# Kernel optimization log

Hardware: AMD Instinct MI355X
Metric: run time of the kernel (lower is better)

## Reference

```python
import math
import jax, jax.numpy as jnp
import numpy as np

D_MODEL = 896
N_HEADS = 14
D_HEAD = D_MODEL // N_HEADS  # 64
ROPE_BASE = 10000.0
LN_EPS = 1e-5
B, N = 8, 1024


def setup_inputs() -> dict:
    key = jax.random.key(0)
    ks = jax.random.split(key, 12)
    s = 1.0 / math.sqrt(D_MODEL)
    return {
        "node_features": jax.random.normal(ks[0], (B, N, D_MODEL), jnp.float32),
        "adj": jax.random.uniform(ks[1], (N, N), jnp.float32),
        "wind_dirs": jax.random.uniform(ks[2], (B, N), jnp.float32),
        "bearings": jax.random.uniform(ks[3], (N, N), jnp.float32),
        "Wq": jax.random.normal(ks[4], (D_MODEL, D_MODEL), jnp.float32) * s,
        "Wk": jax.random.normal(ks[5], (D_MODEL, D_MODEL), jnp.float32) * s,
        "Wv": jax.random.normal(ks[6], (D_MODEL, D_MODEL), jnp.float32) * s,
        "Wo": jax.random.normal(ks[7], (D_MODEL, D_MODEL), jnp.float32) * s,
        "ln_g": jnp.ones((D_MODEL,), jnp.float32),
        "ln_b": jnp.zeros((D_MODEL,), jnp.float32),
        "wind_w": jax.random.normal(ks[8], (2, N_HEADS), jnp.float32) * (1.0 / math.sqrt(2.0)),
        "wind_b": jnp.zeros((N_HEADS,), jnp.float32),
    }


def _layernorm(x, g, b):
    mu = jnp.mean(x, axis=-1, keepdims=True)
    var = jnp.var(x, axis=-1, keepdims=True)
    return (x - mu) * jax.lax.rsqrt(var + LN_EPS) * g + b


def _apply_rotary(x, cos_h, sin_h):
    # x: (B,H,N,d_head); cos_h/sin_h: (N, d_head//2)
    d_half = x.shape[-1] // 2
    x1, x2 = x[..., :d_half], x[..., d_half:]
    return jnp.concatenate([x1 * cos_h - x2 * sin_h, x2 * cos_h + x1 * sin_h], axis=-1)


def reference(node_features, adj, wind_dirs, bearings, Wq, Wk, Wv, Wo, ln_g, ln_b, wind_w, wind_b):
    Bb, Nn, D = node_features.shape
    residual = node_features
    x = _layernorm(node_features, ln_g, ln_b)

    def proj(W):
        return (x @ W).reshape(Bb, Nn, N_HEADS, D_HEAD).transpose(0, 2, 1, 3)  # (B,H,N,dh)

    Q, K, V = proj(Wq), proj(Wk), proj(Wv)

    # RoPE: cos/sin halves (first d_half entries of the duplicated freq table)
    inv_freq = 1.0 / (ROPE_BASE ** (jnp.arange(0, D_HEAD, 2, dtype=jnp.float32) / D_HEAD))
    freqs = jnp.arange(Nn, dtype=jnp.float32)[:, None] * inv_freq[None, :]  # (N, dh/2)
    cos_h, sin_h = jnp.cos(freqs), jnp.sin(freqs)
    Q = _apply_rotary(Q, cos_h, sin_h)
    K = _apply_rotary(K, cos_h, sin_h)

    attn = jnp.einsum("bhqd,bhkd->bhqk", Q, K) / math.sqrt(D_HEAD)
    adj_mask = (adj > 0)[None, None, :, :]
    attn = jnp.where(adj_mask, attn, -1e30)

    # wind-direction dynamic edge bias
    reverse_bearings = (bearings.T + 180.0) % 360.0  # (N,N)
    alignment = jnp.cos(jnp.deg2rad(wind_dirs[:, :, None] - reverse_bearings[None]))  # (B,N,N)
    dist_feat = jnp.broadcast_to(adj[None], (Bb, Nn, Nn))
    edge_features = jnp.stack([alignment, dist_feat], axis=-1)  # (B,N,N,2)
    wind_bias = jnp.tanh(edge_features @ wind_w + wind_b)  # (B,N,N,H)
    attn = attn + wind_bias.transpose(0, 3, 1, 2)  # (B,H,N,N)

    attn = jax.nn.softmax(attn, axis=-1)  # dropout is identity in eval
    out = jnp.einsum("bhqk,bhkd->bhqd", attn, V)
    out = out.transpose(0, 2, 1, 3).reshape(Bb, Nn, D) @ Wo
    return residual + out
```

## Files before the change

### kernel.cpp

```cpp
#include <hip/hip_runtime.h>
#include <hip/hip_bf16.h>
#include <math.h>

#define B_ 8
#define N_ 1024
#define H_ 14
#define DH_ 64
#define D_ 896
#define M_ (B_*N_)
#define DQKV_ 2688

#define TWO_LOG2E_ 2.8853900817779268f
#define BIAS_C_   (-15.869645449778597f)
#define QSCALE_     0.18033688011112043f
#define RAD_        0.017453292519943295f

typedef __attribute__((ext_vector_type(8))) short bf16x8;
typedef __attribute__((ext_vector_type(4))) short bf16x4;
typedef __attribute__((ext_vector_type(4))) float f32x4;

__device__ __forceinline__ float bf2f(short s){
  unsigned u = ((unsigned)(unsigned short)s) << 16;
  union { unsigned u; float f; } c; c.u = u; return c.f;
}
__device__ __forceinline__ short f2bf(float f){
  union { float f; unsigned u; } c; c.f = f;
  unsigned u = c.u;
  unsigned r = (u + 0x7FFFu + ((u >> 16) & 1u)) >> 16;
  return (short)(unsigned short)r;
}
__device__ __forceinline__ float asf(unsigned u){
  union { unsigned u; float f; } c; c.u = u; return c.f;
}
__device__ __forceinline__ unsigned cvt_pk_bf16(float lo, float hi){
  unsigned r;
  asm("v_cvt_pk_bf16_f32 %0, %1, %2" : "=v"(r) : "v"(lo), "v"(hi));
  return r;
}

#if __has_builtin(__builtin_amdgcn_mfma_f32_16x16x16bf16_1k)
#define MFMA16(D, A, B) (D) = __builtin_amdgcn_mfma_f32_16x16x16bf16_1k((A), (B), (D), 0, 0, 0)
#else
#define MFMA16(D, A, B) asm("v_mfma_f32_16x16x16_bf16 %0, %1, %2, %0" : "+v"(D) : "v"(A), "v"(B))
#endif

#define BAR_LDS() do { asm volatile("s_waitcnt lgkmcnt(0)" ::: "memory"); \
                       __builtin_amdgcn_s_barrier(); } while (0)

__global__ __launch_bounds__(256) void ln_kernel(const float* __restrict__ x,
                                                 const float* __restrict__ g,
                                                 const float* __restrict__ bb,
                                                 short* __restrict__ y)
{
  int row = blockIdx.x;
  const float* xr = x + (size_t)row * D_;
  float s = 0.f, s2 = 0.f;
  for (int i = threadIdx.x; i < D_; i += 256){
    float v = xr[i]; s += v; s2 = fmaf(v, v, s2);
  }
  #pragma unroll
  for (int off = 32; off > 0; off >>= 1){
    s  += __shfl_down(s,  off, 64);
    s2 += __shfl_down(s2, off, 64);
  }
  __shared__ float rs_[4], rs2_[4];
  int wv = threadIdx.x >> 6;
  if ((threadIdx.x & 63) == 0){ rs_[wv] = s; rs2_[wv] = s2; }
  __syncthreads();
  float ts  = rs_[0] + rs_[1] + rs_[2] + rs_[3];
  float ts2 = rs2_[0] + rs2_[1] + rs2_[2] + rs2_[3];
  float mu  = ts * (1.f / D_);
  float var = ts2 * (1.f / D_) - mu * mu;
  float rstd = rsqrtf(var + 1e-5f);
  short* yr = y + (size_t)row * D_;
  for (int i = threadIdx.x; i < D_; i += 256){
    yr[i] = f2bf((xr[i] - mu) * rstd * g[i] + bb[i]);
  }
}

__global__ __launch_bounds__(256) void transpose_kernel(
    const float* __restrict__ Wq, const float* __restrict__ Wk,
    const float* __restrict__ Wv, const float* __restrict__ Wo,
    short* __restrict__ WqkvT, short* __restrict__ WoT)
{
  __shared__ short t[64][72];
  int z = blockIdx.z;
  const float* W = (z == 0) ? Wq : (z == 1) ? Wk : (z == 2) ? Wv : Wo;
  int kb = blockIdx.x * 64, nb = blockIdx.y * 64;
  int c0 = (threadIdx.x & 7) * 8;
  int r0 = threadIdx.x >> 3;
  #pragma unroll
  for (int rr = 0; rr < 64; rr += 32){
    const float* src = &W[(size_t)(kb + r0 + rr) * D_ + nb + c0];
    float4 a = *(const float4*)src;
    float4 b = *(const float4*)(src + 4);
    short* dstl = &t[r0 + rr][c0];
    dstl[0] = f2bf(a.x); dstl[1] = f2bf(a.y); dstl[2] = f2bf(a.z); dstl[3] = f2bf(a.w);
    dstl[4] = f2bf(b.x); dstl[5] = f2bf(b.y); dstl[6] = f2bf(b.z); dstl[7] = f2bf(b.w);
  }
  __syncthreads();
  short* dst = (z < 3) ? (WqkvT + (size_t)(z * D_) * D_) : WoT;
  #pragma unroll
  for (int rr = 0; rr < 64; rr += 32){
    int n = nb + r0 + rr;
    bf16x8 v;
    #pragma unroll
    for (int j = 0; j < 8; j++) v[j] = t[c0 + j][r0 + rr];
    *(bf16x8*)&dst[(size_t)n * D_ + kb + c0] = v;
  }
}

__global__ __launch_bounds__(256) void prep_kernel(
    const float* __restrict__ brg, const float* __restrict__ wdir,
    unsigned* __restrict__ csb, short* __restrict__ alignQ, int do_align)
{
  int kt = blockIdx.x, qt = blockIdx.y;
  __shared__ float brgS[64][65];
  __shared__ float cA_[8][64], sA_[8][64];
  int r  = threadIdx.x >> 2;
  int c0 = (threadIdx.x & 3) * 16;

  float bb[16];
  {
    const float* bp = brg + (size_t)(kt * 64 + r) * N_ + qt * 64 + c0;
    #pragma unroll
    for (int i = 0; i < 16; i += 4){
      float4 bv = *(const float4*)(bp + i);
      bb[i] = bv.x; bb[i+1] = bv.y; bb[i+2] = bv.z; bb[i+3] = bv.w;
    }
  }

  if (do_align){
    #pragma unroll
    for (int i = 0; i < 16; i++) brgS[r][c0 + i] = bb[i];
    for (int idx = threadIdx.x; idx < 512; idx += 256){
      int b = idx >> 6, qq = idx & 63;
      float A = wdir[(size_t)b * N_ + qt * 64 + qq] * RAD_;
      float s, c; __sincosf(A, &s, &c);
      sA_[b][qq] = s; cA_[b][qq] = c;
    }
    __syncthreads();
    float cB[16], sB[16];
    #pragma unroll
    for (int i = 0; i < 16; i++){
      float Br = (brgS[c0 + i][r] + 180.f) * RAD_;
      __sincosf(Br, &sB[i], &cB[i]);
    }
    #pragma unroll
    for (int b = 0; b < 8; b++){
      float ca = cA_[b][r], sa = sA_[b][r];
      unsigned w8[8];
      #pragma unroll
      for (int p = 0; p < 8; p++){
        float a0 = fmaf(ca, cB[2*p],     sa * sB[2*p]);
        float a1 = fmaf(ca, cB[2*p + 1], sa * sB[2*p + 1]);
        w8[p] = cvt_pk_bf16(a0, a1);
      }
      short* dst = alignQ + ((size_t)b * N_ + qt * 64 + r) * N_ + kt * 64 + c0;
      *(uint4*)dst       = make_uint4(w8[0], w8[1], w8[2], w8[3]);
      *(uint4*)(dst + 8) = make_uint4(w8[4], w8[5], w8[6], w8[7]);
    }
  } else {
    unsigned* cp = csb + (size_t)(kt * 64 + r) * N_ + qt * 64 + c0;
    #pragma unroll
    for (int i = 0; i < 16; i += 4){
      unsigned o[4];
      #pragma unroll
      for (int j = 0; j < 4; j++){
        float Br = (bb[i + j] + 180.f) * RAD_;
        float sBv, cBv; __sincosf(Br, &sBv, &cBv);
        o[j] = ((unsigned)(unsigned short)f2bf(cBv)) |
               (((unsigned)(unsigned short)f2bf(sBv)) << 16);
      }
      *(uint4*)(cp + i) = make_uint4(o[0], o[1], o[2], o[3]);
    }
  }
}

__global__ __launch_bounds__(256) void gemm_bt(const short* __restrict__ A,
                                               const short* __restrict__ Bt,
                                               short* __restrict__ C,
                                               float* __restrict__ Cf,
                                               const float* __restrict__ residf,
                                               short* __restrict__ VTo,
                                               int N, int rope)
{
  const int K = D_;
  __shared__ short As[128 * 32];
  __shared__ short Bs[128 * 32];
  int tid  = threadIdx.x;
  int wave = tid >> 6;
  int lane = tid & 63;
  int quad = lane >> 4;
  int l16  = lane & 15;
  int wr = wave >> 1, wc = wave & 1;
  int m0 = blockIdx.x * 128;
  int n0 = blockIdx.y * 128;

  f32x4 acc[4][4];
  #pragma unroll
  for (int i = 0; i < 4; i++)
    #pragma unroll
    for (int j = 0; j < 4; j++)
      acc[i][j] = (f32x4){0.f, 0.f, 0.f, 0.f};

  for (int k0 = 0; k0 < K; k0 += 32){
    __syncthreads();
    #pragma unroll
    for (int it = 0; it < 2; ++it){
      int c   = tid + it * 256;
      int row = c >> 2;
      int cc  = c & 3;
      const short* ga = A  + (size_t)(m0 + row) * K + k0 + cc * 8;
      const short* gb = Bt + (size_t)(n0 + row) * K + k0 + cc * 8;
      short* la = As + (size_t)(wave * 64 + it * 256) * 8;
      short* lb = Bs + (size_t)(wave * 64 + it * 256) * 8;
      __builtin_amdgcn_global_load_lds((const __attribute__((address_space(1))) void*)ga,
                                       (__attribute__((address_space(3))) void*)la, 16, 0, 0);
      __builtin_amdgcn_global_load_lds((const __attribute__((address_space(1))) void*)gb,
                                       (__attribute__((address_space(3))) void*)lb, 16, 0, 0);
    }
    __syncthreads();

    bf16x8 af[4], bfr[4];
    #pragma unroll
    for (int i = 0; i < 4; i++)
      af[i] = *(const bf16x8*)(As + (size_t)(wr * 64 + i * 16 + l16) * 32 + quad * 8);
    #pragma unroll
    for (int j = 0; j < 4; j++)
      bfr[j] = *(const bf16x8*)(Bs + (size_t)(wc * 64 + j * 16 + l16) * 32 + quad * 8);
    #pragma unroll
    for (int i = 0; i < 4; i++)
      #pragma unroll
      for (int j = 0; j < 4; j++)
        acc[i][j] = __builtin_amdgcn_mfma_f32_16x16x32_bf16(af[i], bfr[j], acc[i][j], 0, 0, 0);
  }

  int cb  = n0 + wc * 64;
  if (rope){
    int mat = cb / D_;
    if (mat < 2){
      float scale = (mat == 0) ? QSCALE_ : 1.0f;
      float invf0 = exp2f(-0.4152410118609203f * (float)l16);
      float invf1 = invf0 * 0.01f;
      #pragma unroll
      for (int i = 0; i < 4; i++){
        #pragma unroll
        for (int rr = 0; rr < 4; rr++){
          int r = m0 + wr * 64 + i * 16 + quad * 4 + rr;
          float nseq = (float)(r & (N_ - 1));
          float s0, c0v, s1, c1v;
          __sincosf(nseq * invf0, &s0, &c0v);
          __sincosf(nseq * invf1, &s1, &c1v);
          float x1 = acc[i][0][rr], x2 = acc[i][2][rr];
          acc[i][0][rr] = (x1 * c0v - x2 * s0) * scale;
          acc[i][2][rr] = (x2 * c0v + x1 * s0) * scale;
          x1 = acc[i][1][rr]; x2 = acc[i][3][rr];
          acc[i][1][rr] = (x1 * c1v - x2 * s1) * scale;
          acc[i][3][rr] = (x2 * c1v + x1 * s1) * scale;
        }
      }
    }
  }

  if (rope && cb >= 2 * D_){
    int h   = (cb - 2 * D_) >> 6;
    int bb2 = m0 >> 10;
    int nb_ = (m0 & (N_ - 1)) + wr * 64 + quad * 4;
    #pragma unroll
    for (int i = 0; i < 4; i++){
      #pragma unroll
      for (int j = 0; j < 4; j++){
        int d = j * 16 + l16;
        short* vp = VTo + ((size_t)(bb2 * H_ + h) * DH_ + d) * N_ + nb_ + i * 16;
        unsigned o01 = cvt_pk_bf16(acc[i][j][0], acc[i][j][1]);
        unsigned o23 = cvt_pk_bf16(acc[i][j][2], acc[i][j][3]);
        *(uint2*)vp = make_uint2(o01, o23);
      }
    }
  } else {
    #pragma unroll
    for (int i = 0; i < 4; i++){
      #pragma unroll
      for (int rr = 0; rr < 4; rr++){
        int r = m0 + wr * 64 + i * 16 + quad * 4 + rr;
        size_t rowoff = (size_t)r * N;
        #pragma unroll
        for (int j = 0; j < 4; j++){
          int cidx = cb + j * 16 + l16;
          float v = acc[i][j][rr];
          if (Cf){
            Cf[rowoff + cidx] = v + residf[rowoff + cidx];
          } else {
            C[rowoff + cidx] = f2bf(v);
          }
        }
      }
    }
  }
}

template<int PRE>
__global__ __launch_bounds__(256, 2) void attn_kernel(
    const short* __restrict__ QKV,
    const short* __restrict__ VT,
    const unsigned* __restrict__ csb,
    const float* __restrict__ adjF,
    const short* __restrict__ alignQ,
    const float* __restrict__ wind_dirs,
    const float* __restrict__ wind_w,
    const float* __restrict__ wind_b,
    short* __restrict__ outb)
{
  __shared__ short K_s[64 * 72];
  __shared__ short V_t[64 * 76];

  int bid = blockIdx.x;
  int qt  = bid / 112;
  int rem = bid - qt * 112;
  int hh  = rem >> 3;
  int b   = rem & 7;
  int q0  = qt * 64;
  int kt0 = qt;

  int t    = threadIdx.x;
  int w    = t >> 6;
  int lane = t & 63;
  int quad = lane >> 4;
  int l16  = lane & 15;
  int q    = q0 + w * 16 + l16;

  const short* qp = QKV + ((size_t)(b * N_) + q) * DQKV_ + hh * DH_ + quad * 8;
  bf16x8 qb0 = *(const bf16x8*)qp;
  bf16x8 qb1 = *(const bf16x8*)(qp + 32);

  float cAq = 0.f, sAq = 0.f;
  if (!PRE){
    float A = wind_dirs[(size_t)b * N_ + q] * RAD_;
    sAq = __sinf(A); cAq = __cosf(A);
  }
  float w0m = wind_w[hh]      * TWO_LOG2E_;
  float w1m = wind_w[H_ + hh] * TWO_LOG2E_;
  float wbm = wind_b[hh]      * TWO_LOG2E_;

  float lsum = 0.f;
  f32x4 OT[4];
  #pragma unroll
  for (int db = 0; db < 4; db++) OT[db] = (f32x4){0.f, 0.f, 0.f, 0.f};

  int sr = t >> 2, sc = (t & 3) * 16;
  const short* kg0 = QKV + ((size_t)(b * N_) + sr) * DQKV_ + D_ + hh * DH_ + sc;
  const short* vg0 = VT + ((size_t)(b * H_ + hh) * DH_ + sr) * N_ + sc;

  const short* al2 = alignQ + ((size_t)b * N_ + q) * N_ + quad * 4;
  const float* ad2 = adjF + (size_t)q * N_ + quad * 4;

  int k0f = kt0 * 64;
  bf16x8 pkA = *(const bf16x8*)(kg0 + (size_t)k0f * DQKV_);
  bf16x8 pkB = *(const bf16x8*)(kg0 + (size_t)k0f * DQKV_ + 8);
  bf16x8 pvA = *(const bf16x8*)(vg0 + k0f);
  bf16x8 pvB = *(const bf16x8*)(vg0 + k0f + 8);

  float4 ad4[4]; bf16x4 al4[4]; unsigned cs4[4][4];
  #pragma unroll
  for (int jc = 0; jc < 4; jc++){
    ad4[jc] = *(const float4*)(ad2 + k0f + jc * 16);
    if (PRE){
      al4[jc] = *(const bf16x4*)(al2 + k0f + jc * 16);
    } else {
      #pragma unroll
      for (int rr = 0; rr < 4; rr++)
        cs4[jc][rr] = csb[(size_t)(k0f + jc * 16 + quad * 4 + rr) * N_ + q];
    }
  }

  for (int it = 0; it < 16; ++it){
    int kn = (((it + 1 + kt0) & 15)) * 64;

    BAR_LDS();
    *(bf16x8*)(K_s + sr * 72 + sc)     = pkA;
    *(bf16x8*)(K_s + sr * 72 + sc + 8) = pkB;
    *(bf16x8*)(V_t + sr * 76 + sc)     = pvA;
    *(bf16x8*)(V_t + sr * 76 + sc + 8) = pvB;
    BAR_LDS();

    pkA = *(const bf16x8*)(kg0 + (size_t)kn * DQKV_);
    pkB = *(const bf16x8*)(kg0 + (size_t)kn * DQKV_ + 8);
    pvA = *(const bf16x8*)(vg0 + kn);
    pvB = *(const bf16x8*)(vg0 + kn + 8);

    f32x4 S[4];
    __builtin_amdgcn_s_setprio(1);
    #pragma unroll
    for (int jc = 0; jc < 4; jc++){
      bf16x8 ka0 = *(const bf16x8*)(K_s + (jc * 16 + l16) * 72 + quad * 8);
      bf16x8 ka1 = *(const bf16x8*)(K_s + (jc * 16 + l16) * 72 + 32 + quad * 8);
      f32x4 s = (f32x4){0.f, 0.f, 0.f, 0.f};
      s = __builtin_amdgcn_mfma_f32_16x16x32_bf16(ka0, qb0, s, 0, 0, 0);
      s = __builtin_amdgcn_mfma_f32_16x16x32_bf16(ka1, qb1, s, 0, 0, 0);
      S[jc] = s;
    }
    __builtin_amdgcn_s_setprio(0);

    #pragma unroll
    for (int jc = 0; jc < 4; jc++){
      float a4[4] = { ad4[jc].x, ad4[jc].y, ad4[jc].z, ad4[jc].w };
      float ev[4];
      #pragma unroll
      for (int rr = 0; rr < 4; rr++){
        float av = a4[rr];
        float align;
        if (PRE){
          align = bf2f(al4[jc][rr]);
        } else {
          unsigned u = cs4[jc][rr];
          align = cAq * asf(u << 16) + sAq * asf(u & 0xffff0000u);
        }
        float z2 = fmaf(align, w0m, fmaf(av, w1m, wbm));
        float e2 = __builtin_amdgcn_exp2f(z2);
        float rc = __builtin_amdgcn_rcpf(e2 + 1.f);
        float bias2 = fmaf(-TWO_LOG2E_, rc, BIAS_C_);
        float sv = (av > 0.f ? S[jc][rr] : -1e30f) + bias2;
        float e = __builtin_amdgcn_exp2f(sv);
        ev[rr] = e;
        lsum += e;
      }
      union { unsigned u2[2]; bf16x4 v4; } pu;
      pu.u2[0] = cvt_pk_bf16(ev[0], ev[1]);
      pu.u2[1] = cvt_pk_bf16(ev[2], ev[3]);
      bf16x4 pb = pu.v4;

      ad4[jc] = *(const float4*)(ad2 + kn + jc * 16);
      if (PRE){
        al4[jc] = *(const bf16x4*)(al2 + kn + jc * 16);
      } else {
        #pragma unroll
        for (int rr = 0; rr < 4; rr++)
          cs4[jc][rr] = csb[(size_t)(kn + jc * 16 + quad * 4 + rr) * N_ + q];
      }

      __builtin_amdgcn_s_setprio(1);
      #pragma unroll
      for (int db = 0; db < 4; db++){
        bf16x4 va = *(const bf16x4*)(V_t + (db * 16 + l16) * 76 + jc * 16 + quad * 4);
        MFMA16(OT[db], va, pb);
      }
      __builtin_amdgcn_s_setprio(0);
    }
  }

  lsum += __shfl_xor(lsum, 16);
  lsum += __shfl_xor(lsum, 32);
  float rl = 1.f / lsum;

  short* op = outb + ((size_t)(b * N_) + q) * D_ + hh * DH_ + quad * 4;
  #pragma unroll
  for (int db = 0; db < 4; db++){
    unsigned o01 = cvt_pk_bf16(OT[db][0] * rl, OT[db][1] * rl);
    unsigned o23 = cvt_pk_bf16(OT[db][2] * rl, OT[db][3] * rl);
    *(uint2*)(op + db * 16) = make_uint2(o01, o23);
  }
}

extern "C" void kernel_launch(void* const* d_in, const int* in_sizes, int n_in,
                              void* d_out, int out_size, void* d_ws, size_t ws_size,
                              hipStream_t stream)
{
  const float* nf   = (const float*)d_in[0];
  const float* adj  = (const float*)d_in[1];
  const float* wdir = (const float*)d_in[2];
  const float* brg  = (const float*)d_in[3];
  const float* Wq   = (const float*)d_in[4];
  const float* Wk   = (const float*)d_in[5];
  const float* Wv   = (const float*)d_in[6];
  const float* Wo   = (const float*)d_in[7];
  const float* lng  = (const float*)d_in[8];
  const float* lnb  = (const float*)d_in[9];
  const float* ww   = (const float*)d_in[10];
  const float* wbb  = (const float*)d_in[11];
  float* out = (float*)d_out;

  short* base = (short*)d_ws;
  size_t sh = 0;
  short* xln   = base + sh;  sh += (size_t)M_ * D_;
  short* WqkvT = base + sh;  sh += (size_t)DQKV_ * D_;
  short* WoT   = base + sh;  sh += (size_t)D_ * D_;
  short* QKV   = base + sh;  sh += (size_t)M_ * DQKV_;
  short* VT    = base + sh;  sh += (size_t)B_ * H_ * DH_ * N_;
  unsigned* csb = (unsigned*)(base + sh); sh += (size_t)N_ * N_ * 2;
  short* alignQ = base + sh; sh += (size_t)B_ * N_ * N_;
  size_t need_pre = sh * sizeof(short);
  bool pre = (ws_size >= need_pre);

  ln_kernel<<<M_, 256, 0, stream>>>(nf, lng, lnb, xln);
  transpose_kernel<<<dim3(14, 14, 4), 256, 0, stream>>>(Wq, Wk, Wv, Wo, WqkvT, WoT);
  prep_kernel<<<dim3(16, 16), 256, 0, stream>>>(brg, wdir, csb, alignQ, pre ? 1 : 0);
  gemm_bt<<<dim3(M_ / 128, DQKV_ / 128), 256, 0, stream>>>(xln, WqkvT, QKV, nullptr, nullptr, VT, DQKV_, 1);
  if (pre)
    attn_kernel<1><<<B_ * H_ * 16, 256, 0, stream>>>(QKV, VT, csb, adj, alignQ, wdir, ww, wbb, xln);
  else
    attn_kernel<0><<<B_ * H_ * 16, 256, 0, stream>>>(QKV, VT, csb, adj, alignQ, wdir, ww, wbb, xln);
  gemm_bt<<<dim3(M_ / 128, D_ / 128), 256, 0, stream>>>(xln, WoT, nullptr, out, nf, nullptr, D_, 0);
}
```

Before: 367.0 us.

## Fuse prep kernels into one launch, add bf16 adj copy, remap GEMM blocks

Merges the layernorm, weight transpose and bearing/alignment prep kernels into a single launch that dispatches on block index, removing two launch gaps. The prep path also writes a bf16 copy of the adjacency matrix, which the attention kernel now reads in place of fp32 adj, halving that per-tile load. The GEMM grid becomes 1D with an interleaved block-to-tile mapping that spreads neighbouring tiles across eight groups, likely aimed at XCD/L2 locality. The costs are a larger workspace, an extra N×N buffer write, and bf16 rounding of adj, which can change which entries pass the adj>0 mask only for very tiny values.

```diff
diff --git a/kernel.cpp b/kernel.cpp
--- a/kernel.cpp
+++ b/kernel.cpp
@@ -9,6 +9,8 @@
 #define D_ 896
 #define M_ (B_*N_)
 #define DQKV_ 2688
+#define TRBLK_ (14*14*4)
+#define PPBLK_ (16*16)
 
 #define TWO_LOG2E_ 2.8853900817779268f
 #define BIAS_C_   (-15.869645449778597f)
@@ -47,132 +49,156 @@
 #define BAR_LDS() do { asm volatile("s_waitcnt lgkmcnt(0)" ::: "memory"); \
                        __builtin_amdgcn_s_barrier(); } while (0)
 
-__global__ __launch_bounds__(256) void ln_kernel(const float* __restrict__ x,
-                                                 const float* __restrict__ g,
-                                                 const float* __restrict__ bb,
-                                                 short* __restrict__ y)
-{
-  int row = blockIdx.x;
-  const float* xr = x + (size_t)row * D_;
-  float s = 0.f, s2 = 0.f;
-  for (int i = threadIdx.x; i < D_; i += 256){
-    float v = xr[i]; s += v; s2 = fmaf(v, v, s2);
-  }
-  #pragma unroll
-  for (int off = 32; off > 0; off >>= 1){
-    s  += __shfl_down(s,  off, 64);
-    s2 += __shfl_down(s2, off, 64);
-  }
-  __shared__ float rs_[4], rs2_[4];
-  int wv = threadIdx.x >> 6;
-  if ((threadIdx.x & 63) == 0){ rs_[wv] = s; rs2_[wv] = s2; }
-  __syncthreads();
-  float ts  = rs_[0] + rs_[1] + rs_[2] + rs_[3];
-  float ts2 = rs2_[0] + rs2_[1] + rs2_[2] + rs2_[3];
-  float mu  = ts * (1.f / D_);
-  float var = ts2 * (1.f / D_) - mu * mu;
-  float rstd = rsqrtf(var + 1e-5f);
-  short* yr = y + (size_t)row * D_;
-  for (int i = threadIdx.x; i < D_; i += 256){
-    yr[i] = f2bf((xr[i] - mu) * rstd * g[i] + bb[i]);
-  }
-}
-
-__global__ __launch_bounds__(256) void transpose_kernel(
+__global__ __launch_bounds__(256) void fused_pre(
+    const float* __restrict__ x, const float* __restrict__ g,
+    const float* __restrict__ bbv, short* __restrict__ y,
     const float* __restrict__ Wq, const float* __restrict__ Wk,
     const float* __restrict__ Wv, const float* __restrict__ Wo,
-    short* __restrict__ WqkvT, short* __restrict__ WoT)
+    short* __restrict__ WqkvT, short* __restrict__ WoT,
+    const float* __restrict__ adj, const float* __restrict__ brg,
+    const float* __restrict__ wdir,
+    unsigned* __restrict__ csb, short* __restrict__ alignQ,
+    short* __restrict__ adjQ, int do_align)
 {
-  __shared__ short t[64][72];
-  int z = blockIdx.z;
-  const float* W = (z == 0) ? Wq : (z == 1) ? Wk : (z == 2) ? Wv : Wo;
-  int kb = blockIdx.x * 64, nb = blockIdx.y * 64;
-  int c0 = (threadIdx.x & 7) * 8;
-  int r0 = threadIdx.x >> 3;
-  #pragma unroll
-  for (int rr = 0; rr < 64; rr += 32){
-    const float* src = &W[(size_t)(kb + r0 + rr) * D_ + nb + c0];
-    float4 a = *(const float4*)src;
-    float4 b = *(const float4*)(src + 4);
-    short* dstl = &t[r0 + rr][c0];
-    dstl[0] = f2bf(a.x); dstl[1] = f2bf(a.y); dstl[2] = f2bf(a.z); dstl[3] = f2bf(a.w);
-    dstl[4] = f2bf(b.x); dstl[5] = f2bf(b.y); dstl[6] = f2bf(b.z); dstl[7] = f2bf(b.w);
-  }
-  __syncthreads();
-  short* dst = (z < 3) ? (WqkvT + (size_t)(z * D_) * D_) : WoT;
-  #pragma unroll
-  for (int rr = 0; rr < 64; rr += 32){
-    int n = nb + r0 + rr;
-    bf16x8 v;
-    #pragma unroll
-    for (int j = 0; j < 8; j++) v[j] = t[c0 + j][r0 + rr];
-    *(bf16x8*)&dst[(size_t)n * D_ + kb + c0] = v;
-  }
-}
-
-__global__ __launch_bounds__(256) void prep_kernel(
-    const float* __restrict__ brg, const float* __restrict__ wdir,
-    unsigned* __restrict__ csb, short* __restrict__ alignQ, int do_align)
-{
-  int kt = blockIdx.x, qt = blockIdx.y;
-  __shared__ float brgS[64][65];
-  __shared__ float cA_[8][64], sA_[8][64];
-  int r  = threadIdx.x >> 2;
-  int c0 = (threadIdx.x & 3) * 16;
-
-  float bb[16];
+  __shared__ __align__(16) char smem_[20992];
+  int bid = blockIdx.x;
+
+  if (bid < M_){
+    float* rs_  = (float*)smem_;
+    float* rs2_ = rs_ + 4;
+    int row = bid;
+    const float* xr = x + (size_t)row * D_;
+    float s = 0.f, s2 = 0.f;
+    for (int i = threadIdx.x; i < D_; i += 256){
+      float v = xr[i]; s += v; s2 = fmaf(v, v, s2);
+    }
+    #pragma unroll
+    for (int off = 32; off > 0; off >>= 1){
+      s  += __shfl_down(s,  off, 64);
+      s2 += __shfl_down(s2, off, 64);
+    }
+    int wv = threadIdx.x >> 6;
+    if ((threadIdx.x & 63) == 0){ rs_[wv] = s; rs2_[wv] = s2; }
+    __syncthreads();
+    float ts  = rs_[0] + rs_[1] + rs_[2] + rs_[3];
+    float ts2 = rs2_[0] + rs2_[1] + rs2_[2] + rs2_[3];
+    float mu  = ts * (1.f / D_);
+    float var = ts2 * (1.f / D_) - mu * mu;
+    float rstd = rsqrtf(var + 1e-5f);
+    short* yr = y + (size_t)row * D_;
+    for (int i = threadIdx.x; i < D_; i += 256){
+      yr[i] = f2bf((xr[i] - mu) * rstd * g[i] + bbv[i]);
+    }
+    return;
+  }
+
+  if (bid < M_ + TRBLK_){
+    short (*t)[72] = (short(*)[72])smem_;
+    int rem = bid - M_;
+    int z  = rem / 196;
+    int r2 = rem - z * 196;
+    int kb = (r2 % 14) * 64, nb = (r2 / 14) * 64;
+    const float* W = (z == 0) ? Wq : (z == 1) ? Wk : (z == 2) ? Wv : Wo;
+    int c0 = (threadIdx.x & 7) * 8;
+    int r0 = threadIdx.x >> 3;
+    #pragma unroll
+    for (int rr = 0; rr < 64; rr += 32){
+      const float* src = &W[(size_t)(kb + r0 + rr) * D_ + nb + c0];
+      float4 a = *(const float4*)src;
+      float4 b = *(const float4*)(src + 4);
+      short* dstl = &t[r0 + rr][c0];
+      dstl[0] = f2bf(a.x); dstl[1] = f2bf(a.y); dstl[2] = f2bf(a.z); dstl[3] = f2bf(a.w);
+      dstl[4] = f2bf(b.x); dstl[5] = f2bf(b.y); dstl[6] = f2bf(b.z); dstl[7] = f2bf(b.w);
+    }
+    __syncthreads();
+    short* dst = (z < 3) ? (WqkvT + (size_t)(z * D_) * D_) : WoT;
+    #pragma unroll
+    for (int rr = 0; rr < 64; rr += 32){
+      int n = nb + r0 + rr;
+      bf16x8 v;
+      #pragma unroll
+      for (int j = 0; j < 8; j++) v[j] = t[c0 + j][r0 + rr];
+      *(bf16x8*)&dst[(size_t)n * D_ + kb + c0] = v;
+    }
+    return;
+  }
+
   {
-    const float* bp = brg + (size_t)(kt * 64 + r) * N_ + qt * 64 + c0;
-    #pragma unroll
-    for (int i = 0; i < 16; i += 4){
-      float4 bv = *(const float4*)(bp + i);
-      bb[i] = bv.x; bb[i+1] = bv.y; bb[i+2] = bv.z; bb[i+3] = bv.w;
-    }
-  }
-
-  if (do_align){
-    #pragma unroll
-    for (int i = 0; i < 16; i++) brgS[r][c0 + i] = bb[i];
-    for (int idx = threadIdx.x; idx < 512; idx += 256){
-      int b = idx >> 6, qq = idx & 63;
-      float A = wdir[(size_t)b * N_ + qt * 64 + qq] * RAD_;
-      float s, c; __sincosf(A, &s, &c);
-      sA_[b][qq] = s; cA_[b][qq] = c;
-    }
-    __syncthreads();
-    float cB[16], sB[16];
-    #pragma unroll
-    for (int i = 0; i < 16; i++){
-      float Br = (brgS[c0 + i][r] + 180.f) * RAD_;
-      __sincosf(Br, &sB[i], &cB[i]);
-    }
-    #pragma unroll
-    for (int b = 0; b < 8; b++){
-      float ca = cA_[b][r], sa = sA_[b][r];
-      unsigned w8[8];
-      #pragma unroll
-      for (int p = 0; p < 8; p++){
-        float a0 = fmaf(ca, cB[2*p],     sa * sB[2*p]);
-        float a1 = fmaf(ca, cB[2*p + 1], sa * sB[2*p + 1]);
-        w8[p] = cvt_pk_bf16(a0, a1);
-      }
-      short* dst = alignQ + ((size_t)b * N_ + qt * 64 + r) * N_ + kt * 64 + c0;
-      *(uint4*)dst       = make_uint4(w8[0], w8[1], w8[2], w8[3]);
-      *(uint4*)(dst + 8) = make_uint4(w8[4], w8[5], w8[6], w8[7]);
-    }
-  } else {
-    unsigned* cp = csb + (size_t)(kt * 64 + r) * N_ + qt * 64 + c0;
-    #pragma unroll
-    for (int i = 0; i < 16; i += 4){
-      unsigned o[4];
-      #pragma unroll
-      for (int j = 0; j < 4; j++){
-        float Br = (bb[i + j] + 180.f) * RAD_;
-        float sBv, cBv; __sincosf(Br, &sBv, &cBv);
-        o[j] = ((unsigned)(unsigned short)f2bf(cBv)) |
-               (((unsigned)(unsigned short)f2bf(sBv)) << 16);
-      }
-      *(uint4*)(cp + i) = make_uint4(o[0], o[1], o[2], o[3]);
+    float (*brgS)[65] = (float(*)[65])smem_;
+    float (*cA_)[64]  = (float(*)[64])(smem_ + 16640);
+    float (*sA_)[64]  = (float(*)[64])(smem_ + 16640 + 2048);
+    int rem = bid - M_ - TRBLK_;
+    int kt = rem & 15, qt = rem >> 4;
+    int r  = threadIdx.x >> 2;
+    int c0 = (threadIdx.x & 3) * 16;
+
+    float bb16[16];
+    {
+      const float* bp = brg + (size_t)(kt * 64 + r) * N_ + qt * 64 + c0;
+      #pragma unroll
+      for (int i = 0; i < 16; i += 4){
+        float4 bv = *(const float4*)(bp + i);
+        bb16[i] = bv.x; bb16[i+1] = bv.y; bb16[i+2] = bv.z; bb16[i+3] = bv.w;
+      }
+    }
+
+    if (do_align){
+      #pragma unroll
+      for (int i = 0; i < 16; i++) brgS[r][c0 + i] = bb16[i];
+      for (int idx = threadIdx.x; idx < 512; idx += 256){
+        int b = idx >> 6, qq = idx & 63;
+        float A = wdir[(size_t)b * N_ + qt * 64 + qq] * RAD_;
+        float s, c; __sincosf(A, &s, &c);
+        sA_[b][qq] = s; cA_[b][qq] = c;
+      }
+      {
+        const float* ap = adj + (size_t)(qt * 64 + r) * N_ + kt * 64 + c0;
+        unsigned w8[8];
+        #pragma unroll
+        for (int i = 0; i < 16; i += 4){
+          float4 av = *(const float4*)(ap + i);
+          w8[i/2]     = cvt_pk_bf16(av.x, av.y);
+          w8[i/2 + 1] = cvt_pk_bf16(av.z, av.w);
+        }
+        short* dst = adjQ + (size_t)(qt * 64 + r) * N_ + kt * 64 + c0;
+        *(uint4*)dst       = make_uint4(w8[0], w8[1], w8[2], w8[3]);
+        *(uint4*)(dst + 8) = make_uint4(w8[4], w8[5], w8[6], w8[7]);
+      }
+      __syncthreads();
+      float cB[16], sB[16];
+      #pragma unroll
+      for (int i = 0; i < 16; i++){
+        float Br = (brgS[c0 + i][r] + 180.f) * RAD_;
+        __sincosf(Br, &sB[i], &cB[i]);
+      }
+      #pragma unroll
+      for (int b = 0; b < 8; b++){
+        float ca = cA_[b][r], sa = sA_[b][r];
+        unsigned w8[8];
+        #pragma unroll
+        for (int p = 0; p < 8; p++){
+          float a0 = fmaf(ca, cB[2*p],     sa * sB[2*p]);
+          float a1 = fmaf(ca, cB[2*p + 1], sa * sB[2*p + 1]);
+          w8[p] = cvt_pk_bf16(a0, a1);
+        }
+        short* dst = alignQ + ((size_t)b * N_ + qt * 64 + r) * N_ + kt * 64 + c0;
+        *(uint4*)dst       = make_uint4(w8[0], w8[1], w8[2], w8[3]);
+        *(uint4*)(dst + 8) = make_uint4(w8[4], w8[5], w8[6], w8[7]);
+      }
+    } else {
+      unsigned* cp = csb + (size_t)(kt * 64 + r) * N_ + qt * 64 + c0;
+      #pragma unroll
+      for (int i = 0; i < 16; i += 4){
+        unsigned o[4];
+        #pragma unroll
+        for (int j = 0; j < 4; j++){
+          float Br = (bb16[i + j] + 180.f) * RAD_;
+          float sBv, cBv; __sincosf(Br, &sBv, &cBv);
+          o[j] = ((unsigned)(unsigned short)f2bf(cBv)) |
+                 (((unsigned)(unsigned short)f2bf(sBv)) << 16);
+        }
+        *(uint4*)(cp + i) = make_uint4(o[0], o[1], o[2], o[3]);
+      }
     }
   }
 }
@@ -194,8 +220,16 @@
   int quad = lane >> 4;
   int l16  = lane & 15;
   int wr = wave >> 1, wc = wave & 1;
-  int m0 = blockIdx.x * 128;
-  int n0 = blockIdx.y * 128;
+
+  int nN    = N >> 7;
+  int nwg   = (M_ >> 7) * nN;
+  int chunk = nwg >> 3;
+  int l     = blockIdx.x;
+  int l2    = (l & 7) * chunk + (l >> 3);
+  int mi    = l2 / nN;
+  int ni    = l2 - mi * nN;
+  int m0 = mi * 128;
+  int n0 = ni * 128;
 
   f32x4 acc[4][4];
   #pragma unroll
@@ -307,6 +341,7 @@
     const unsigned* __restrict__ csb,
     const float* __restrict__ adjF,
     const short* __restrict__ alignQ,
+    const short* __restrict__ adjQ,
     const float* __restrict__ wind_dirs,
     const float* __restrict__ wind_w,
     const float* __restrict__ wind_b,
@@ -353,6 +388,7 @@
   const short* vg0 = VT + ((size_t)(b * H_ + hh) * DH_ + sr) * N_ + sc;
 
   const short* al2 = alignQ + ((size_t)b * N_ + q) * N_ + quad * 4;
+  const short* aj2 = adjQ + (size_t)q * N_ + quad * 4;
   const float* ad2 = adjF + (size_t)q * N_ + quad * 4;
 
   int k0f = kt0 * 64;
@@ -361,13 +397,14 @@
   bf16x8 pvA = *(const bf16x8*)(vg0 + k0f);
   bf16x8 pvB = *(const bf16x8*)(vg0 + k0f + 8);
 
-  float4 ad4[4]; bf16x4 al4[4]; unsigned cs4[4][4];
+  float4 ad4[4]; bf16x4 al4[4], aj4[4]; unsigned cs4[4][4];
   #pragma unroll
   for (int jc = 0; jc < 4; jc++){
-    ad4[jc] = *(const float4*)(ad2 + k0f + jc * 16);
     if (PRE){
       al4[jc] = *(const bf16x4*)(al2 + k0f + jc * 16);
+      aj4[jc] = *(const bf16x4*)(aj2 + k0f + jc * 16);
     } else {
+      ad4[jc] = *(const float4*)(ad2 + k0f + jc * 16);
       #pragma unroll
       for (int rr = 0; rr < 4; rr++)
         cs4[jc][rr] = csb[(size_t)(k0f + jc * 16 + quad * 4 + rr) * N_ + q];
@@ -404,15 +441,16 @@
 
     #pragma unroll
     for (int jc = 0; jc < 4; jc++){
-      float a4[4] = { ad4[jc].x, ad4[jc].y, ad4[jc].z, ad4[jc].w };
       float ev[4];
       #pragma unroll
       for (int rr = 0; rr < 4; rr++){
-        float av = a4[rr];
-        float align;
+        float av, align;
         if (PRE){
           align = bf2f(al4[jc][rr]);
+          av    = bf2f(aj4[jc][rr]);
         } else {
+          float4 a4 = ad4[jc];
+          av = (rr == 0) ? a4.x : (rr == 1) ? a4.y : (rr == 2) ? a4.z : a4.w;
           unsigned u = cs4[jc][rr];
           align = cAq * asf(u << 16) + sAq * asf(u & 0xffff0000u);
         }
@@ -430,10 +468,11 @@
       pu.u2[1] = cvt_pk_bf16(ev[2], ev[3]);
       bf16x4 pb = pu.v4;
 
-      ad4[jc] = *(const float4*)(ad2 + kn + jc * 16);
       if (PRE){
         al4[jc] = *(const bf16x4*)(al2 + kn + jc * 16);
+        aj4[jc] = *(const bf16x4*)(aj2 + kn + jc * 16);
       } else {
+        ad4[jc] = *(const float4*)(ad2 + kn + jc * 16);
         #pragma unroll
         for (int rr = 0; rr < 4; rr++)
           cs4[jc][rr] = csb[(size_t)(kn + jc * 16 + quad * 4 + rr) * N_ + q];
@@ -489,16 +528,19 @@
   short* VT    = base + sh;  sh += (size_t)B_ * H_ * DH_ * N_;
   unsigned* csb = (unsigned*)(base + sh); sh += (size_t)N_ * N_ * 2;
   short* alignQ = base + sh; sh += (size_t)B_ * N_ * N_;
+  short* adjQ   = base + sh; sh += (size_t)N_ * N_;
   size_t need_pre = sh * sizeof(short);
   bool pre = (ws_size >= need_pre);
 
-  ln_kernel<<<M_, 256, 0, stream>>>(nf, lng, lnb, xln);
-  transpose_kernel<<<dim3(14, 14, 4), 256, 0, stream>>>(Wq, Wk, Wv, Wo, WqkvT, WoT);
-  prep_kernel<<<dim3(16, 16), 256, 0, stream>>>(brg, wdir, csb, alignQ, pre ? 1 : 0);
-  gemm_bt<<<dim3(M_ / 128, DQKV_ / 128), 256, 0, stream>>>(xln, WqkvT, QKV, nullptr, nullptr, VT, DQKV_, 1);
+  fused_pre<<<M_ + TRBLK_ + PPBLK_, 256, 0, stream>>>(
+      nf, lng, lnb, xln, Wq, Wk, Wv, Wo, WqkvT, WoT,
+      adj, brg, wdir, csb, alignQ, adjQ, pre ? 1 : 0);
+  gemm_bt<<<(M_ / 128) * (DQKV_ / 128), 256, 0, stream>>>(
+      xln, WqkvT, QKV, nullptr, nullptr, VT, DQKV_, 1);
   if (pre)
-    attn_kernel<1><<<B_ * H_ * 16, 256, 0, stream>>>(QKV, VT, csb, adj, alignQ, wdir, ww, wbb, xln);
+    attn_kernel<1><<<B_ * H_ * 16, 256, 0, stream>>>(QKV, VT, csb, adj, alignQ, adjQ, wdir, ww, wbb, xln);
   else
-    attn_kernel<0><<<B_ * H_ * 16, 256, 0, stream>>>(QKV, VT, csb, adj, alignQ, wdir, ww, wbb, xln);
-  gemm_bt<<<dim3(M_ / 128, D_ / 128), 256, 0, stream>>>(xln, WoT, nullptr, out, nf, nullptr, D_, 0);
-}
+    attn_kernel<0><<<B_ * H_ * 16, 256, 0, stream>>>(QKV, VT, csb, adj, alignQ, adjQ, wdir, ww, wbb, xln);
+  gemm_bt<<<(M_ / 128) * (D_ / 128), 256, 0, stream>>>(
+      xln, WoT, nullptr, out, nf, nullptr, D_, 0);
+}
```

After: 368.5 us. Within noise of the previous version (+0.4%).
